# Performance work log

Hardware: AMD Instinct MI355X
Metric: run time of the kernel (lower is better)

The kernel has to match this reference:

```python
import jax, jax.numpy as jnp
import numpy as np

E, F, H = 8, 5632, 2048
T = 8192


def setup_inputs() -> dict:
    key = jax.random.key(0)
    k1, k2, k3, k4 = jax.random.split(key, 4)
    s_w = 1.0 / np.sqrt(H)
    return {
        "expert_idx": 3,
        "hidden_states": jax.random.normal(k1, (T, H), dtype=jnp.float32),
        "fc1_1": jax.random.normal(k2, (E, F, H), dtype=jnp.float32) * s_w,
        "fc1_2": jax.random.normal(k3, (E, F, H), dtype=jnp.float32) * s_w,
        "fc2": jax.random.normal(k4, (E, H, F), dtype=jnp.float32) * (1.0 / np.sqrt(F)),
    }


def reference(expert_idx, hidden_states, fc1_1, fc1_2, fc2):
    # Select this expert's weights: [F,H], [F,H], [H,F]
    w1 = fc1_1[expert_idx]
    w2 = fc1_2[expert_idx]
    w3 = fc2[expert_idx]
    # SwiGLU FFN: silu(x @ w1^T) * (x @ w2^T) @ w3^T
    gate = jnp.einsum("th,fh->tf", hidden_states, w1)
    up = jnp.einsum("th,fh->tf", hidden_states, w2)
    fc1_out = jax.nn.silu(gate) * up  # [T, F]
    out = jnp.einsum("tf,hf->th", fc1_out, w3)  # [T, H]
    return out
```

## Files before the change

kernel.cpp:

```cpp
#include <hip/hip_runtime.h>
#include <hip/hip_bf16.h>

#define T_DIM 8192
#define H_DIM 2048
#define F_DIM 5632

typedef __attribute__((ext_vector_type(4))) float f32x4;
typedef __attribute__((ext_vector_type(8))) short bf16x8;

static __device__ __forceinline__ void gload16(const void* g, void* l) {
    __builtin_amdgcn_global_load_lds(
        (const __attribute__((address_space(1))) void*)g,
        (__attribute__((address_space(3))) void*)l,
        16, 0, 0);
}

static __device__ __forceinline__ unsigned short f2bf(float f) {
    unsigned int u = __float_as_uint(f);
    u += 0x7fffu + ((u >> 16) & 1u);
    return (unsigned short)(u >> 16);
}

__global__ __launch_bounds__(256)
void cvt_f32_bf16(const float* __restrict__ base, const int* __restrict__ eidx,
                  long per_expert, unsigned short* __restrict__ dst, long n)
{
    const float* src = base;
    if (eidx) src += (long)(*eidx) * per_expert;
    const long stride = (long)gridDim.x * blockDim.x;
    for (long i = (long)blockIdx.x * blockDim.x + threadIdx.x; i * 4 < n; i += stride) {
        const float4 v = *(const float4*)(src + i * 4);
        ushort4 o;
        o.x = f2bf(v.x); o.y = f2bf(v.y); o.z = f2bf(v.z); o.w = f2bf(v.w);
        *(ushort4*)(dst + i * 4) = o;
    }
}

__global__ __launch_bounds__(256, 2)
void gemm1_swiglu(const unsigned short* __restrict__ X,
                  const unsigned short* __restrict__ W1,
                  const unsigned short* __restrict__ W2,
                  unsigned short* __restrict__ Hout)
{
    __shared__ __align__(16) unsigned short sA [128 * 64];
    __shared__ __align__(16) unsigned short sB1[128 * 64];
    __shared__ __align__(16) unsigned short sB2[128 * 64];

    const int tid  = threadIdx.x;
    const int lane = tid & 63;
    const int wid  = tid >> 6;
    const int wm   = wid >> 1;
    const int wn   = wid & 1;
    const int bm   = blockIdx.y;
    const int bn   = blockIdx.x;

    const int  srow = wid * 32 + (lane >> 3);
    const int  scol = (lane & 7) * 8;
    const long gA0  = (long)(bm * 128 + srow) * H_DIM + scol;
    const long gB0  = (long)(bn * 128 + srow) * H_DIM + scol;
    const int  lds0 = wid * 2048;

    const int arow = wm * 64 + (lane & 15);
    const int brow = wn * 64 + (lane & 15);
    const int koff = (lane >> 4) * 8;

    f32x4 accg[4][4] = {};
    f32x4 accu[4][4] = {};

    for (int kt = 0; kt < H_DIM / 64; ++kt) {
        __syncthreads();
        const int kb = kt * 64;
        #pragma unroll
        for (int i = 0; i < 4; ++i) {
            const long go = (long)i * (8 * H_DIM);
            const int  lo = lds0 + i * 512;
            gload16(X  + gA0 + go + kb, sA  + lo);
            gload16(W1 + gB0 + go + kb, sB1 + lo);
            gload16(W2 + gB0 + go + kb, sB2 + lo);
        }
        __syncthreads();
        #pragma unroll
        for (int kk = 0; kk < 2; ++kk) {
            bf16x8 af[4], b1f[4], b2f[4];
            const int ko = kk * 32 + koff;
            #pragma unroll
            for (int mi = 0; mi < 4; ++mi)
                af[mi] = *(const bf16x8*)(sA + (arow + mi * 16) * 64 + ko);
            #pragma unroll
            for (int ni = 0; ni < 4; ++ni) {
                b1f[ni] = *(const bf16x8*)(sB1 + (brow + ni * 16) * 64 + ko);
                b2f[ni] = *(const bf16x8*)(sB2 + (brow + ni * 16) * 64 + ko);
            }
            #pragma unroll
            for (int mi = 0; mi < 4; ++mi)
                #pragma unroll
                for (int ni = 0; ni < 4; ++ni) {
                    accg[mi][ni] = __builtin_amdgcn_mfma_f32_16x16x32_bf16(
                        af[mi], b1f[ni], accg[mi][ni], 0, 0, 0);
                    accu[mi][ni] = __builtin_amdgcn_mfma_f32_16x16x32_bf16(
                        af[mi], b2f[ni], accu[mi][ni], 0, 0, 0);
                }
        }
    }

    const int orow0 = bm * 128 + wm * 64 + ((lane >> 4) << 2);
    const int ocol0 = bn * 128 + wn * 64 + (lane & 15);
    #pragma unroll
    for (int mi = 0; mi < 4; ++mi)
        #pragma unroll
        for (int ni = 0; ni < 4; ++ni) {
            const f32x4 g = accg[mi][ni];
            const f32x4 u = accu[mi][ni];
            #pragma unroll
            for (int r = 0; r < 4; ++r) {
                const float gv = g[r];
                const float hv = (gv / (1.0f + __expf(-gv))) * u[r];
                Hout[(long)(orow0 + mi * 16 + r) * F_DIM + (ocol0 + ni * 16)] = f2bf(hv);
            }
        }
}

__global__ __launch_bounds__(256, 2)
void gemm2_out(const unsigned short* __restrict__ A,
               const unsigned short* __restrict__ B,
               float* __restrict__ Out)
{
    __shared__ __align__(16) unsigned short sA[128 * 64];
    __shared__ __align__(16) unsigned short sB[128 * 64];

    const int tid  = threadIdx.x;
    const int lane = tid & 63;
    const int wid  = tid >> 6;
    const int wm   = wid >> 1;
    const int wn   = wid & 1;
    const int bm   = blockIdx.y;
    const int bn   = blockIdx.x;

    const int  srow = wid * 32 + (lane >> 3);
    const int  scol = (lane & 7) * 8;
    const long gA0  = (long)(bm * 128 + srow) * F_DIM + scol;
    const long gB0  = (long)(bn * 128 + srow) * F_DIM + scol;
    const int  lds0 = wid * 2048;

    const int arow = wm * 64 + (lane & 15);
    const int brow = wn * 64 + (lane & 15);
    const int koff = (lane >> 4) * 8;

    f32x4 acc[4][4] = {};

    for (int kt = 0; kt < F_DIM / 64; ++kt) {
        __syncthreads();
        const int kb = kt * 64;
        #pragma unroll
        for (int i = 0; i < 4; ++i) {
            const long go = (long)i * (8 * F_DIM);
            const int  lo = lds0 + i * 512;
            gload16(A + gA0 + go + kb, sA + lo);
            gload16(B + gB0 + go + kb, sB + lo);
        }
        __syncthreads();
        #pragma unroll
        for (int kk = 0; kk < 2; ++kk) {
            bf16x8 af[4], bf[4];
            const int ko = kk * 32 + koff;
            #pragma unroll
            for (int mi = 0; mi < 4; ++mi)
                af[mi] = *(const bf16x8*)(sA + (arow + mi * 16) * 64 + ko);
            #pragma unroll
            for (int ni = 0; ni < 4; ++ni)
                bf[ni] = *(const bf16x8*)(sB + (brow + ni * 16) * 64 + ko);
            #pragma unroll
            for (int mi = 0; mi < 4; ++mi)
                #pragma unroll
                for (int ni = 0; ni < 4; ++ni)
                    acc[mi][ni] = __builtin_amdgcn_mfma_f32_16x16x32_bf16(
                        af[mi], bf[ni], acc[mi][ni], 0, 0, 0);
        }
    }

    const int orow0 = bm * 128 + wm * 64 + ((lane >> 4) << 2);
    const int ocol0 = bn * 128 + wn * 64 + (lane & 15);
    #pragma unroll
    for (int mi = 0; mi < 4; ++mi)
        #pragma unroll
        for (int ni = 0; ni < 4; ++ni) {
            const f32x4 c = acc[mi][ni];
            #pragma unroll
            for (int r = 0; r < 4; ++r)
                Out[(long)(orow0 + mi * 16 + r) * H_DIM + (ocol0 + ni * 16)] = c[r];
        }
}

extern "C" void kernel_launch(void* const* d_in, const int* in_sizes, int n_in,
                              void* d_out, int out_size, void* d_ws, size_t ws_size,
                              hipStream_t stream)
{
    const int*   eidx = (const int*)d_in[0];
    const float* x    = (const float*)d_in[1];
    const float* w1   = (const float*)d_in[2];
    const float* w2   = (const float*)d_in[3];
    const float* w3   = (const float*)d_in[4];
    float* out = (float*)d_out;

    unsigned short* Xb  = (unsigned short*)d_ws;
    unsigned short* W1b = Xb  + (long)T_DIM * H_DIM;
    unsigned short* W2b = W1b + (long)F_DIM * H_DIM;
    unsigned short* W3b = W2b + (long)F_DIM * H_DIM;
    unsigned short* Hb  = W3b + (long)H_DIM * F_DIM;

    cvt_f32_bf16<<<2048, 256, 0, stream>>>(x,  nullptr, 0, Xb, (long)T_DIM * H_DIM);
    cvt_f32_bf16<<<2048, 256, 0, stream>>>(w1, eidx, (long)F_DIM * H_DIM, W1b, (long)F_DIM * H_DIM);
    cvt_f32_bf16<<<2048, 256, 0, stream>>>(w2, eidx, (long)F_DIM * H_DIM, W2b, (long)F_DIM * H_DIM);
    cvt_f32_bf16<<<2048, 256, 0, stream>>>(w3, eidx, (long)H_DIM * F_DIM, W3b, (long)H_DIM * F_DIM);

    gemm1_swiglu<<<dim3(F_DIM / 128, T_DIM / 128), 256, 0, stream>>>(Xb, W1b, W2b, Hb);
    gemm2_out  <<<dim3(H_DIM / 128, T_DIM / 128), 256, 0, stream>>>(Hb, W3b, out);
}
```

Before: 660.5 us.

## Rewrite both GEMMs with 256-wide tiles, double-buffered swizzled LDS and XCD block remap

Both GEMM kernels move to 512-thread blocks that compute 256x256 tiles. Global-to-LDS loads are double-buffered and interleaved with MFMA phases under s_setprio, and the LDS layout is XOR-swizzled to avoid bank conflicts. In gemm1, W1 and W2 rows are stacked into a single B tile, so half of the waves compute the gate and half compute the up projection. The up results pass through LDS to the gate waves for the SwiGLU epilogue. Block indices are remapped across the 8 XCDs for L2 locality, and the 128KB of LDS per block limits occupancy to one block per CU.

```diff
diff --git a/kernel.cpp b/kernel.cpp
--- a/kernel.cpp
+++ b/kernel.cpp
@@ -36,159 +36,213 @@
     }
 }
 
-__global__ __launch_bounds__(256, 2)
+static __device__ __forceinline__ void stage_half(const unsigned short* __restrict__ g,
+                                                  long grow0, long ldk, long kb,
+                                                  unsigned short* l, int t, int i0)
+{
+    const int r  = t >> 3;
+    const int cc = ((t & 7) ^ (r & 7)) << 3;
+    #pragma unroll
+    for (int i = i0; i < i0 + 2; ++i)
+        gload16(g + (grow0 + i * 64 + r) * ldk + kb + cc,
+                l + i * 4096 + t * 8);
+}
+
+static __device__ __forceinline__ bf16x8 ldsfrag(const unsigned short* base,
+                                                 int row, int kk, int q)
+{
+    return *(const bf16x8*)(base + row * 64 + (((kk * 4 + q) ^ (row & 7)) << 3));
+}
+
+#define PHASE_BODY(p, STAGE_STMT)                                              \
+    {                                                                          \
+        bf16x8 af[2][2];                                                       \
+        _Pragma("unroll")                                                      \
+        for (int l_ = 0; l_ < 2; ++l_)                                         \
+            _Pragma("unroll")                                                  \
+            for (int kk = 0; kk < 2; ++kk)                                     \
+                af[l_][kk] = ldsfrag(la, wm * 128 + (p) * 32 + l_ * 16 + lr, kk, q); \
+        STAGE_STMT;                                                            \
+        __builtin_amdgcn_s_barrier();                                          \
+        __builtin_amdgcn_s_setprio(1);                                         \
+        _Pragma("unroll")                                                      \
+        for (int l_ = 0; l_ < 2; ++l_)                                         \
+            _Pragma("unroll")                                                  \
+            for (int ni = 0; ni < 4; ++ni)                                     \
+                _Pragma("unroll")                                              \
+                for (int kk = 0; kk < 2; ++kk)                                 \
+                    acc[(p) * 2 + l_][ni] = __builtin_amdgcn_mfma_f32_16x16x32_bf16( \
+                        af[l_][kk], bf[ni][kk], acc[(p) * 2 + l_][ni], 0, 0, 0);     \
+        __builtin_amdgcn_s_setprio(0);                                         \
+        __builtin_amdgcn_s_barrier();                                          \
+    }
+
+__global__ __launch_bounds__(512, 2)
 void gemm1_swiglu(const unsigned short* __restrict__ X,
                   const unsigned short* __restrict__ W1,
                   const unsigned short* __restrict__ W2,
                   unsigned short* __restrict__ Hout)
 {
-    __shared__ __align__(16) unsigned short sA [128 * 64];
-    __shared__ __align__(16) unsigned short sB1[128 * 64];
-    __shared__ __align__(16) unsigned short sB2[128 * 64];
+    __shared__ __align__(16) unsigned short sAll[4 * 16384];
 
     const int tid  = threadIdx.x;
     const int lane = tid & 63;
     const int wid  = tid >> 6;
-    const int wm   = wid >> 1;
-    const int wn   = wid & 1;
-    const int bm   = blockIdx.y;
-    const int bn   = blockIdx.x;
-
-    const int  srow = wid * 32 + (lane >> 3);
-    const int  scol = (lane & 7) * 8;
-    const long gA0  = (long)(bm * 128 + srow) * H_DIM + scol;
-    const long gB0  = (long)(bn * 128 + srow) * H_DIM + scol;
-    const int  lds0 = wid * 2048;
-
-    const int arow = wm * 64 + (lane & 15);
-    const int brow = wn * 64 + (lane & 15);
-    const int koff = (lane >> 4) * 8;
-
-    f32x4 accg[4][4] = {};
-    f32x4 accu[4][4] = {};
-
-    for (int kt = 0; kt < H_DIM / 64; ++kt) {
-        __syncthreads();
-        const int kb = kt * 64;
-        #pragma unroll
-        for (int i = 0; i < 4; ++i) {
-            const long go = (long)i * (8 * H_DIM);
-            const int  lo = lds0 + i * 512;
-            gload16(X  + gA0 + go + kb, sA  + lo);
-            gload16(W1 + gB0 + go + kb, sB1 + lo);
-            gload16(W2 + gB0 + go + kb, sB2 + lo);
+    const int wm   = wid >> 2;
+    const int wn   = wid & 3;
+    const int q    = lane >> 4;
+    const int lr   = lane & 15;
+
+    const int nwg = gridDim.x;
+    const int bid = blockIdx.x;
+    const int cpx = nwg >> 3;
+    const int swz = (bid & 7) * cpx + (bid >> 3);
+    const int NBN = F_DIM / 128;
+    const int bm  = swz / NBN;
+    const int bn  = swz % NBN;
+
+    const long arow0 = (long)bm * 256;
+    const long b1r0  = (long)bn * 128;
+    const long b2r0  = (long)bn * 128 - 128;
+    const int  NK    = H_DIM / 64;
+
+    f32x4 acc[8][4] = {};
+
+    stage_half(X,  arow0, H_DIM, 0, sAll,          tid, 0);
+    stage_half(X,  arow0, H_DIM, 0, sAll,          tid, 2);
+    stage_half(W1, b1r0,  H_DIM, 0, sAll + 16384,  tid, 0);
+    stage_half(W2, b2r0,  H_DIM, 0, sAll + 16384,  tid, 2);
+    stage_half(W1, b1r0,  H_DIM, 64, sAll + 49152, tid, 0);
+    stage_half(W2, b2r0,  H_DIM, 64, sAll + 49152, tid, 2);
+
+    for (int j = 0; j < NK; ++j) {
+        unsigned short* la = sAll + (j & 1) * 32768;
+        unsigned short* lb = la + 16384;
+
+        if (j + 1 < NK) {
+            unsigned short* na = sAll + ((j + 1) & 1) * 32768;
+            stage_half(X, arow0, H_DIM, (long)(j + 1) * 64, na, tid, 0);
+            stage_half(X, arow0, H_DIM, (long)(j + 1) * 64, na, tid, 2);
+            asm volatile("s_waitcnt vmcnt(8)" ::: "memory");
+        } else {
+            asm volatile("s_waitcnt vmcnt(0)" ::: "memory");
         }
-        __syncthreads();
-        #pragma unroll
-        for (int kk = 0; kk < 2; ++kk) {
-            bf16x8 af[4], b1f[4], b2f[4];
-            const int ko = kk * 32 + koff;
-            #pragma unroll
-            for (int mi = 0; mi < 4; ++mi)
-                af[mi] = *(const bf16x8*)(sA + (arow + mi * 16) * 64 + ko);
-            #pragma unroll
-            for (int ni = 0; ni < 4; ++ni) {
-                b1f[ni] = *(const bf16x8*)(sB1 + (brow + ni * 16) * 64 + ko);
-                b2f[ni] = *(const bf16x8*)(sB2 + (brow + ni * 16) * 64 + ko);
-            }
-            #pragma unroll
-            for (int mi = 0; mi < 4; ++mi)
+        __builtin_amdgcn_s_barrier();
+
+        bf16x8 bf[4][2];
+        #pragma unroll
+        for (int ni = 0; ni < 4; ++ni)
+            #pragma unroll
+            for (int kk = 0; kk < 2; ++kk)
+                bf[ni][kk] = ldsfrag(lb, wn * 64 + ni * 16 + lr, kk, q);
+
+        PHASE_BODY(0, {})
+        PHASE_BODY(1, { if (j + 2 < NK) stage_half(W1, b1r0, H_DIM, (long)(j + 2) * 64, lb, tid, 0); })
+        PHASE_BODY(2, { if (j + 2 < NK) stage_half(W2, b2r0, H_DIM, (long)(j + 2) * 64, lb, tid, 2); })
+        PHASE_BODY(3, {})
+    }
+
+    float* slab = (float*)sAll;
+    float* s = slab + (wm * 2 + (wn & 1)) * 8192;
+    if (wn >= 2) {
+        #pragma unroll
+        for (int mi = 0; mi < 8; ++mi)
+            #pragma unroll
+            for (int ni = 0; ni < 4; ++ni)
                 #pragma unroll
-                for (int ni = 0; ni < 4; ++ni) {
-                    accg[mi][ni] = __builtin_amdgcn_mfma_f32_16x16x32_bf16(
-                        af[mi], b1f[ni], accg[mi][ni], 0, 0, 0);
-                    accu[mi][ni] = __builtin_amdgcn_mfma_f32_16x16x32_bf16(
-                        af[mi], b2f[ni], accu[mi][ni], 0, 0, 0);
+                for (int r = 0; r < 4; ++r)
+                    s[(mi * 16 + q * 4 + r) * 64 + ni * 16 + lr] = acc[mi][ni][r];
+    }
+    __syncthreads();
+    if (wn < 2) {
+        const long orow = (long)bm * 256 + wm * 128;
+        const long ocol = (long)bn * 128 + wn * 64;
+        #pragma unroll
+        for (int mi = 0; mi < 8; ++mi)
+            #pragma unroll
+            for (int ni = 0; ni < 4; ++ni)
+                #pragma unroll
+                for (int r = 0; r < 4; ++r) {
+                    const float g = acc[mi][ni][r];
+                    const float u = s[(mi * 16 + q * 4 + r) * 64 + ni * 16 + lr];
+                    const float h = (g / (1.0f + __expf(-g))) * u;
+                    Hout[(orow + mi * 16 + q * 4 + r) * F_DIM + (ocol + ni * 16 + lr)] = f2bf(h);
                 }
-        }
-    }
-
-    const int orow0 = bm * 128 + wm * 64 + ((lane >> 4) << 2);
-    const int ocol0 = bn * 128 + wn * 64 + (lane & 15);
-    #pragma unroll
-    for (int mi = 0; mi < 4; ++mi)
-        #pragma unroll
-        for (int ni = 0; ni < 4; ++ni) {
-            const f32x4 g = accg[mi][ni];
-            const f32x4 u = accu[mi][ni];
-            #pragma unroll
-            for (int r = 0; r < 4; ++r) {
-                const float gv = g[r];
-                const float hv = (gv / (1.0f + __expf(-gv))) * u[r];
-                Hout[(long)(orow0 + mi * 16 + r) * F_DIM + (ocol0 + ni * 16)] = f2bf(hv);
-            }
-        }
-}
-
-__global__ __launch_bounds__(256, 2)
+    }
+}
+
+__global__ __launch_bounds__(512, 2)
 void gemm2_out(const unsigned short* __restrict__ A,
                const unsigned short* __restrict__ B,
                float* __restrict__ Out)
 {
-    __shared__ __align__(16) unsigned short sA[128 * 64];
-    __shared__ __align__(16) unsigned short sB[128 * 64];
+    __shared__ __align__(16) unsigned short sAll[4 * 16384];
 
     const int tid  = threadIdx.x;
     const int lane = tid & 63;
     const int wid  = tid >> 6;
-    const int wm   = wid >> 1;
-    const int wn   = wid & 1;
-    const int bm   = blockIdx.y;
-    const int bn   = blockIdx.x;
-
-    const int  srow = wid * 32 + (lane >> 3);
-    const int  scol = (lane & 7) * 8;
-    const long gA0  = (long)(bm * 128 + srow) * F_DIM + scol;
-    const long gB0  = (long)(bn * 128 + srow) * F_DIM + scol;
-    const int  lds0 = wid * 2048;
-
-    const int arow = wm * 64 + (lane & 15);
-    const int brow = wn * 64 + (lane & 15);
-    const int koff = (lane >> 4) * 8;
-
-    f32x4 acc[4][4] = {};
-
-    for (int kt = 0; kt < F_DIM / 64; ++kt) {
-        __syncthreads();
-        const int kb = kt * 64;
-        #pragma unroll
-        for (int i = 0; i < 4; ++i) {
-            const long go = (long)i * (8 * F_DIM);
-            const int  lo = lds0 + i * 512;
-            gload16(A + gA0 + go + kb, sA + lo);
-            gload16(B + gB0 + go + kb, sB + lo);
+    const int wm   = wid >> 2;
+    const int wn   = wid & 3;
+    const int q    = lane >> 4;
+    const int lr   = lane & 15;
+
+    const int nwg = gridDim.x;
+    const int bid = blockIdx.x;
+    const int cpx = nwg >> 3;
+    const int swz = (bid & 7) * cpx + (bid >> 3);
+    const int NBN = H_DIM / 256;
+    const int bm  = swz / NBN;
+    const int bn  = swz % NBN;
+
+    const long arow0 = (long)bm * 256;
+    const long brow0 = (long)bn * 256;
+    const int  NK    = F_DIM / 64;
+
+    f32x4 acc[8][4] = {};
+
+    stage_half(A, arow0, F_DIM, 0, sAll,          tid, 0);
+    stage_half(A, arow0, F_DIM, 0, sAll,          tid, 2);
+    stage_half(B, brow0, F_DIM, 0, sAll + 16384,  tid, 0);
+    stage_half(B, brow0, F_DIM, 0, sAll + 16384,  tid, 2);
+    stage_half(B, brow0, F_DIM, 64, sAll + 49152, tid, 0);
+    stage_half(B, brow0, F_DIM, 64, sAll + 49152, tid, 2);
+
+    for (int j = 0; j < NK; ++j) {
+        unsigned short* la = sAll + (j & 1) * 32768;
+        unsigned short* lb = la + 16384;
+
+        if (j + 1 < NK) {
+            unsigned short* na = sAll + ((j + 1) & 1) * 32768;
+            stage_half(A, arow0, F_DIM, (long)(j + 1) * 64, na, tid, 0);
+            stage_half(A, arow0, F_DIM, (long)(j + 1) * 64, na, tid, 2);
+            asm volatile("s_waitcnt vmcnt(8)" ::: "memory");
+        } else {
+            asm volatile("s_waitcnt vmcnt(0)" ::: "memory");
         }
-        __syncthreads();
-        #pragma unroll
-        for (int kk = 0; kk < 2; ++kk) {
-            bf16x8 af[4], bf[4];
-            const int ko = kk * 32 + koff;
-            #pragma unroll
-            for (int mi = 0; mi < 4; ++mi)
-                af[mi] = *(const bf16x8*)(sA + (arow + mi * 16) * 64 + ko);
-            #pragma unroll
-            for (int ni = 0; ni < 4; ++ni)
-                bf[ni] = *(const bf16x8*)(sB + (brow + ni * 16) * 64 + ko);
-            #pragma unroll
-            for (int mi = 0; mi < 4; ++mi)
-                #pragma unroll
-                for (int ni = 0; ni < 4; ++ni)
-                    acc[mi][ni] = __builtin_amdgcn_mfma_f32_16x16x32_bf16(
-                        af[mi], bf[ni], acc[mi][ni], 0, 0, 0);
-        }
-    }
-
-    const int orow0 = bm * 128 + wm * 64 + ((lane >> 4) << 2);
-    const int ocol0 = bn * 128 + wn * 64 + (lane & 15);
+        __builtin_amdgcn_s_barrier();
+
+        bf16x8 bf[4][2];
+        #pragma unroll
+        for (int ni = 0; ni < 4; ++ni)
+            #pragma unroll
+            for (int kk = 0; kk < 2; ++kk)
+                bf[ni][kk] = ldsfrag(lb, wn * 64 + ni * 16 + lr, kk, q);
+
+        PHASE_BODY(0, {})
+        PHASE_BODY(1, { if (j + 2 < NK) stage_half(B, brow0, F_DIM, (long)(j + 2) * 64, lb, tid, 0); })
+        PHASE_BODY(2, { if (j + 2 < NK) stage_half(B, brow0, F_DIM, (long)(j + 2) * 64, lb, tid, 2); })
+        PHASE_BODY(3, {})
+    }
+
+    const long orow = (long)bm * 256 + wm * 128;
+    const long ocol = (long)bn * 256 + wn * 64;
     #pragma unroll
-    for (int mi = 0; mi < 4; ++mi)
-        #pragma unroll
-        for (int ni = 0; ni < 4; ++ni) {
-            const f32x4 c = acc[mi][ni];
+    for (int mi = 0; mi < 8; ++mi)
+        #pragma unroll
+        for (int ni = 0; ni < 4; ++ni)
             #pragma unroll
             for (int r = 0; r < 4; ++r)
-                Out[(long)(orow0 + mi * 16 + r) * H_DIM + (ocol0 + ni * 16)] = c[r];
-        }
+                Out[(orow + mi * 16 + q * 4 + r) * H_DIM + (ocol + ni * 16 + lr)] = acc[mi][ni][r];
 }
 
 extern "C" void kernel_launch(void* const* d_in, const int* in_sizes, int n_in,
@@ -213,6 +267,6 @@
     cvt_f32_bf16<<<2048, 256, 0, stream>>>(w2, eidx, (long)F_DIM * H_DIM, W2b, (long)F_DIM * H_DIM);
     cvt_f32_bf16<<<2048, 256, 0, stream>>>(w3, eidx, (long)H_DIM * F_DIM, W3b, (long)H_DIM * F_DIM);
 
-    gemm1_swiglu<<<dim3(F_DIM / 128, T_DIM / 128), 256, 0, stream>>>(Xb, W1b, W2b, Hb);
-    gemm2_out  <<<dim3(H_DIM / 128, T_DIM / 128), 256, 0, stream>>>(Hb, W3b, out);
-}
+    gemm1_swiglu<<<(T_DIM / 256) * (F_DIM / 128), 512, 0, stream>>>(Xb, W1b, W2b, Hb);
+    gemm2_out  <<<(T_DIM / 256) * (H_DIM / 256), 512, 0, stream>>>(Hb, W3b, out);
+}
```

New measurement: 588.9 us. 1.12x faster.
